# Kernel optimization log

Hardware: AMD Instinct MI355X
Metric: run time of the kernel (lower is better)

## Reference

```python
import jax, jax.numpy as jnp
import numpy as np

S, B, D = 2048, 2, 768
H = 12
DK = D // H
DFF = 3072
EPS = 1e-5


def _layernorm(x, g, b):
    mu = jnp.mean(x, axis=-1, keepdims=True)
    var = jnp.mean(jnp.square(x - mu), axis=-1, keepdims=True)
    return (x - mu) * jax.lax.rsqrt(var + EPS) * g + b


def setup_inputs() -> dict:
    key = jax.random.key(0)
    ks = jax.random.split(key, 12)
    s = 0.02
    return {
        "x": jax.random.normal(ks[0], (S, B, D), jnp.float32),
        "wq": jax.random.normal(ks[1], (D, D), jnp.float32) * s,
        "bq": jnp.zeros((D,), jnp.float32),
        "wk": jax.random.normal(ks[2], (D, D), jnp.float32) * s,
        "bk": jnp.zeros((D,), jnp.float32),
        "wv": jax.random.normal(ks[3], (D, D), jnp.float32) * s,
        "bv": jnp.zeros((D,), jnp.float32),
        "wo": jax.random.normal(ks[4], (D, D), jnp.float32) * s,
        "bo": jnp.zeros((D,), jnp.float32),
        "g1": jnp.ones((D,), jnp.float32),
        "b1": jnp.zeros((D,), jnp.float32),
        "g2": jnp.ones((D,), jnp.float32),
        "b2": jnp.zeros((D,), jnp.float32),
        "w1": jax.random.normal(ks[5], (DFF, D), jnp.float32) * s,
        "bb1": jnp.zeros((DFF,), jnp.float32),
        "w2": jax.random.normal(ks[6], (D, DFF), jnp.float32) * s,
        "bb2": jnp.zeros((D,), jnp.float32),
    }


def reference(x, wq, bq, wk, bk, wv, bv, wo, bo, g1, b1, g2, b2, w1, bb1, w2, bb2):
    scale = 1.0 / np.sqrt(DK)
    # --- pre-norm MHA ---
    z = _layernorm(x, g1, b1)                      # [S,B,D]
    q = (z @ wq.T + bq).reshape(S, B, H, DK)
    k = (z @ wk.T + bk).reshape(S, B, H, DK)
    v = (z @ wv.T + bv).reshape(S, B, H, DK)
    scores = jnp.einsum('ibhd,jbhd->ijbh', q, k) * scale  # [S,S,B,H]
    attn = jax.nn.softmax(scores, axis=1)                  # softmax over keys
    ctx = jnp.einsum('ijbh,jbhd->ibhd', attn, v).reshape(S, B, D)
    a = ctx @ wo.T + bo
    x = x + a
    # --- pre-norm FFN (ELU) ---
    z = _layernorm(x, g2, b2)
    h = jax.nn.elu(z @ w1.T + bb1)
    a = h @ w2.T + bb2
    return x + a
```

## Files before the change

kernel.cpp:

```cpp
#include <hip/hip_runtime.h>
#include <hip/hip_bf16.h>
#include <math.h>

#define S_LEN   2048
#define B_SZ    2
#define D_MODEL 768
#define N_HEADS 12
#define DFF     3072
#define N_TOK   4096
#define EPS     1e-5f
#define QKV_N   2304
#define SLOG2E  0.18033688011112042f
#define NSPLIT  2

typedef __attribute__((ext_vector_type(8))) short short8;
typedef __attribute__((ext_vector_type(4))) float f32x4;
typedef unsigned long long u64;
typedef unsigned short u16;
typedef unsigned u32;

__device__ __forceinline__ void gload16(const void* g, void* l) {
    __builtin_amdgcn_global_load_lds(
        (const __attribute__((address_space(1))) void*)g,
        (__attribute__((address_space(3))) void*)l, 16, 0, 0);
}
__device__ __forceinline__ u16 f2bf(float x) {
    union { float f; unsigned u; } c; c.f = x;
    unsigned r = c.u + 0x7FFF + ((c.u >> 16) & 1);
    return (u16)(r >> 16);
}
__device__ __forceinline__ float bf2f(u16 u) {
    union { unsigned u; float f; } c; c.u = ((unsigned)u) << 16; return c.f;
}
__device__ __forceinline__ float fast_exp2(float x) {
    float r; asm("v_exp_f32 %0, %1" : "=v"(r) : "v"(x)); return r;
}

__global__ __launch_bounds__(256) void cvt_all(
    const float* __restrict__ wq, const float* __restrict__ wk,
    const float* __restrict__ wv, const float* __restrict__ wo,
    const float* __restrict__ w1, const float* __restrict__ w2,
    u16* __restrict__ dst)
{
    const int W = 147456;
    int i = blockIdx.x * 256 + threadIdx.x;
    const float* src; int off;
    if      (i <     W) { src = wq; off = 0;     }
    else if (i < 2 * W) { src = wk; off = W;     }
    else if (i < 3 * W) { src = wv; off = 2 * W; }
    else if (i < 4 * W) { src = wo; off = 3 * W; }
    else if (i < 8 * W) { src = w1; off = 4 * W; }
    else                { src = w2; off = 8 * W; }
    float4 v = ((const float4*)src)[i - off];
    union { u16 u[4]; u64 ll; } o;
    o.u[0] = f2bf(v.x); o.u[1] = f2bf(v.y); o.u[2] = f2bf(v.z); o.u[3] = f2bf(v.w);
    ((u64*)dst)[i] = o.ll;
}

__global__ __launch_bounds__(256) void concat_bias(
    const float* __restrict__ bq, const float* __restrict__ bk,
    const float* __restrict__ bv, float* __restrict__ d)
{
    int i = blockIdx.x * 256 + threadIdx.x;
    if (i < 768) d[i] = bq[i];
    else if (i < 1536) d[i] = bk[i - 768];
    else d[i] = bv[i - 1536];
}

__global__ __launch_bounds__(256) void ln_kernel(
    const float* __restrict__ x, const float* __restrict__ g,
    const float* __restrict__ b, u16* __restrict__ z)
{
    int row = blockIdx.x;
    const float* xr = x + (size_t)row * D_MODEL;
    u16* zr = z + (size_t)row * D_MODEL;
    int t = threadIdx.x;
    float loc[3];
    float s1 = 0.f, s2 = 0.f;
#pragma unroll
    for (int i = 0; i < 3; ++i) {
        float v = xr[t + 256 * i];
        loc[i] = v; s1 += v; s2 += v * v;
    }
#pragma unroll
    for (int off = 32; off > 0; off >>= 1) {
        s1 += __shfl_down(s1, off);
        s2 += __shfl_down(s2, off);
    }
    __shared__ float r1[4], r2[4];
    __shared__ float mu_s, is_s;
    int wave = t >> 6, lane = t & 63;
    if (lane == 0) { r1[wave] = s1; r2[wave] = s2; }
    __syncthreads();
    if (t == 0) {
        float a = r1[0] + r1[1] + r1[2] + r1[3];
        float c = r2[0] + r2[1] + r2[2] + r2[3];
        float mu = a * (1.f / D_MODEL);
        float var = c * (1.f / D_MODEL) - mu * mu;
        mu_s = mu; is_s = rsqrtf(var + EPS);
    }
    __syncthreads();
    float mu = mu_s, istd = is_s;
#pragma unroll
    for (int i = 0; i < 3; ++i) {
        int c = t + 256 * i;
        zr[c] = f2bf((loc[i] - mu) * istd * g[c] + b[c]);
    }
}

__global__ __launch_bounds__(256) void ln_fuse(
    const float* __restrict__ x, const u16* __restrict__ p0,
    const u16* __restrict__ p1, const float* __restrict__ bres,
    const float* __restrict__ g, const float* __restrict__ b,
    float* __restrict__ xout, u16* __restrict__ z)
{
    int row = blockIdx.x;
    const float* xr = x + (size_t)row * D_MODEL;
    const u16* p0r = p0 + (size_t)row * D_MODEL;
    const u16* p1r = p1 + (size_t)row * D_MODEL;
    int t = threadIdx.x;
    float loc[3];
    float s1 = 0.f, s2 = 0.f;
#pragma unroll
    for (int i = 0; i < 3; ++i) {
        int c = t + 256 * i;
        float v = xr[c] + bf2f(p0r[c]) + bf2f(p1r[c]) + bres[c];
        loc[i] = v; s1 += v; s2 += v * v;
    }
#pragma unroll
    for (int off = 32; off > 0; off >>= 1) {
        s1 += __shfl_down(s1, off);
        s2 += __shfl_down(s2, off);
    }
    __shared__ float r1[4], r2[4];
    __shared__ float mu_s, is_s;
    int wave = t >> 6, lane = t & 63;
    if (lane == 0) { r1[wave] = s1; r2[wave] = s2; }
    __syncthreads();
    if (t == 0) {
        float a = r1[0] + r1[1] + r1[2] + r1[3];
        float c = r2[0] + r2[1] + r2[2] + r2[3];
        float mu = a * (1.f / D_MODEL);
        float var = c * (1.f / D_MODEL) - mu * mu;
        mu_s = mu; is_s = rsqrtf(var + EPS);
    }
    __syncthreads();
    float mu = mu_s, istd = is_s;
    float* xo = xout + (size_t)row * D_MODEL;
    u16* zr = z + (size_t)row * D_MODEL;
#pragma unroll
    for (int i = 0; i < 3; ++i) {
        int c = t + 256 * i;
        xo[c] = loc[i];
        zr[c] = f2bf((loc[i] - mu) * istd * g[c] + b[c]);
    }
}

template <int MODE>
__global__ __launch_bounds__(256) void gemm_mfma(
    const u16* __restrict__ A, const u16* __restrict__ W,
    const float* __restrict__ bias, void* __restrict__ outp,
    u16* __restrict__ vt, int Ncols, int K, int lda, int ldw, int koff)
{
    __shared__ short AsB[3][128 * 32];
    __shared__ short BsB[3][128 * 32];

    const int t = threadIdx.x;
    const int lane = t & 63, w = t >> 6;
    const int wr = w >> 1, wc = w & 1;

    const int nwg = gridDim.x * gridDim.y;
    const int bid = blockIdx.y * gridDim.x + blockIdx.x;
    const int wg  = (bid & 7) * (nwg >> 3) + (bid >> 3);
    const int row0 = (wg / gridDim.x) * 128;
    const int col0 = (wg % gridDim.x) * 128;
    const int fr = lane & 15, fg = lane >> 4;

    if (MODE == 4) {
        A += (size_t)blockIdx.z * koff;
        W += (size_t)blockIdx.z * koff;
    }

    int o0 = w * 1024 + lane * 16;
    int r0s = o0 >> 6,          sl0 = (o0 >> 4) & 3;
    int r1s = (o0 + 4096) >> 6, sl1 = ((o0 + 4096) >> 4) & 3;
    int ss0 = sl0 ^ ((r0s >> 1) & 3);
    int ss1 = sl1 ^ ((r1s >> 1) & 3);
    const u16* Asrc0 = A + (size_t)(row0 + r0s) * lda + ss0 * 8;
    const u16* Asrc1 = A + (size_t)(row0 + r1s) * lda + ss1 * 8;
    const u16* Bsrc0 = W + (size_t)(col0 + r0s) * ldw + ss0 * 8;
    const u16* Bsrc1 = W + (size_t)(col0 + r1s) * ldw + ss1 * 8;
    const int od0 = w * 1024, od1 = w * 1024 + 4096;

    f32x4 acc[4][4] = {};
    const int nt = K / 32;

    auto stage = [&](int c, int k0) {
        gload16(Asrc0 + k0, (char*)AsB[c] + od0);
        gload16(Asrc1 + k0, (char*)AsB[c] + od1);
        gload16(Bsrc0 + k0, (char*)BsB[c] + od0);
        gload16(Bsrc1 + k0, (char*)BsB[c] + od1);
    };

    stage(0, 0);
    stage(1, 32);

    for (int tt = 0; tt < nt; ++tt) {
        if (tt + 1 < nt)
            asm volatile("s_waitcnt vmcnt(4)\n\ts_barrier" ::: "memory");
        else
            asm volatile("s_waitcnt vmcnt(0)\n\ts_barrier" ::: "memory");
        if (tt + 2 < nt) stage((tt + 2) % 3, (tt + 2) * 32);

        const char* As = (const char*)AsB[tt % 3];
        const char* Bs = (const char*)BsB[tt % 3];
        short8 af[4], bfr[4];
#pragma unroll
        for (int m = 0; m < 4; ++m) {
            int r = wr * 64 + m * 16 + fr;
            af[m] = *(const short8*)(As + r * 64 + ((fg ^ ((r >> 1) & 3)) << 4));
        }
#pragma unroll
        for (int n = 0; n < 4; ++n) {
            int r = wc * 64 + n * 16 + fr;
            bfr[n] = *(const short8*)(Bs + r * 64 + ((fg ^ ((r >> 1) & 3)) << 4));
        }
#pragma unroll
        for (int m = 0; m < 4; ++m)
#pragma unroll
            for (int n = 0; n < 4; ++n)
                acc[m][n] = __builtin_amdgcn_mfma_f32_16x16x32_bf16(
                    af[m], bfr[n], acc[m][n], 0, 0, 0);
    }

    u16* pout16 = nullptr;
    if (MODE == 4) pout16 = blockIdx.z ? vt : (u16*)outp;

#pragma unroll
    for (int m = 0; m < 4; ++m) {
        int rbase = row0 + wr * 64 + m * 16 + fg * 4;
#pragma unroll
        for (int n = 0; n < 4; ++n) {
            int col = col0 + wc * 64 + n * 16 + fr;
            float bv = (MODE == 4) ? 0.f : bias[col];
            if (MODE == 1 && col >= 1536) {
                int cc = col - 1536, hh = cc >> 6, dk = cc & 63;
                int s_a = rbase >> 1;
                float v0 = acc[m][n][0] + bv, v1 = acc[m][n][1] + bv;
                float v2 = acc[m][n][2] + bv, v3 = acc[m][n][3] + bv;
                unsigned lo = (unsigned)f2bf(v0) | ((unsigned)f2bf(v2) << 16);
                unsigned hi = (unsigned)f2bf(v1) | ((unsigned)f2bf(v3) << 16);
                *(unsigned*)&vt[((size_t)hh * 64 + dk) * 2048 + s_a] = lo;
                *(unsigned*)&vt[((size_t)(N_HEADS + hh) * 64 + dk) * 2048 + s_a] = hi;
            } else {
#pragma unroll
                for (int r = 0; r < 4; ++r) {
                    int row = rbase + r;
                    float v = acc[m][n][r] + bv;
                    if (MODE == 3) {
                        v = v > 0.f ? v : (fast_exp2(v * 1.44269504f) - 1.f);
                        ((u16*)outp)[(size_t)row * Ncols + col] = f2bf(v);
                    } else if (MODE == 4) {
                        pout16[(size_t)row * 768 + col] = f2bf(v);
                    } else {
                        if (col < 768) v *= SLOG2E;
                        ((u16*)outp)[(size_t)row * QKV_N + col] = f2bf(v);
                    }
                }
            }
        }
    }
}

__global__ __launch_bounds__(256) void reduce_add(
    const u16* __restrict__ p0, const u16* __restrict__ p1,
    const float* __restrict__ bias, const float* __restrict__ res,
    float* __restrict__ out)
{
    int i = blockIdx.x * 256 + threadIdx.x;
    int col4 = i % (D_MODEL / 4);
    u64 a = ((const u64*)p0)[i];
    u64 c = ((const u64*)p1)[i];
    float4 o = ((const float4*)res)[i];
    float4 bb = ((const float4*)bias)[col4];
    o.x += bf2f((u16)a)         + bf2f((u16)c)         + bb.x;
    o.y += bf2f((u16)(a >> 16)) + bf2f((u16)(c >> 16)) + bb.y;
    o.z += bf2f((u16)(a >> 32)) + bf2f((u16)(c >> 32)) + bb.z;
    o.w += bf2f((u16)(a >> 48)) + bf2f((u16)(c >> 48)) + bb.w;
    ((float4*)out)[i] = o;
}

__global__ __launch_bounds__(256) void attn_mfma(
    const u16* qkv, const u16* __restrict__ vt,
    u16* op0, u16* __restrict__ op1, float* __restrict__ lp)
{
    __shared__ short KsB[2][64 * 64];
    __shared__ short VtB[2][64 * 64];
    __shared__ short PsB[4][32 * 64];

    const int t = threadIdx.x, lane = t & 63, w = t >> 6;
    const int fr = lane & 15, fg = lane >> 4;
    const int fg4 = fg * 4;

    const int nwg = gridDim.x * gridDim.y;
    const int bid = blockIdx.y * gridDim.x + blockIdx.x;
    const int wg  = (bid & 7) * (nwg >> 3) + (bid >> 3);
    const int qb = wg % gridDim.x, bh = wg / gridDim.x;
    const int zid = blockIdx.z;
    const int b = bh / N_HEADS, h = bh % N_HEADS;

    short8 qf[2][2];
#pragma unroll
    for (int qg = 0; qg < 2; ++qg) {
        int srow = qb * 128 + w * 32 + qg * 16 + fr;
        size_t tok = (size_t)srow * B_SZ + b;
#pragma unroll
        for (int s = 0; s < 2; ++s)
            qf[qg][s] = *(const short8*)(qkv + tok * QKV_N + h * 64 + s * 32 + fg * 8);
    }

    const short8 ones8 = { (short)0x3F80, (short)0x3F80, (short)0x3F80, (short)0x3F80,
                           (short)0x3F80, (short)0x3F80, (short)0x3F80, (short)0x3F80 };

    f32x4 l_acc[2] = {};
    f32x4 O[2][4] = {};

    int o0 = w * 1024 + lane * 16;
    int r0 = o0 >> 7,          sl0 = (o0 >> 4) & 7;
    int r1 = (o0 + 4096) >> 7, sl1 = ((o0 + 4096) >> 4) & 7;
    int ss0 = sl0 ^ (r0 & 7), ss1 = sl1 ^ (r1 & 7);
    const u16* kbase = qkv + 768 + h * 64;
    const u16* vtb = vt + (size_t)bh * 64 * S_LEN;
    const int od0 = w * 1024, od1 = w * 1024 + 4096;
    char* Pw = (char*)PsB[w];

    auto stageKV = [&](int c, int kb) {
        gload16(kbase + ((size_t)(kb * 64 + r0) * B_SZ + b) * QKV_N + ss0 * 8, (char*)KsB[c] + od0);
        gload16(kbase + ((size_t)(kb * 64 + r1) * B_SZ + b) * QKV_N + ss1 * 8, (char*)KsB[c] + od1);
        gload16(vtb + (size_t)r0 * S_LEN + kb * 64 + ss0 * 8, (char*)VtB[c] + od0);
        gload16(vtb + (size_t)r1 * S_LEN + kb * 64 + ss1 * 8, (char*)VtB[c] + od1);
    };

    const int kb0 = zid * (S_LEN / 64 / NSPLIT);
    stageKV(0, kb0);

    for (int it = 0; it < S_LEN / 64 / NSPLIT; ++it) {
        __syncthreads();
        if (it + 1 < S_LEN / 64 / NSPLIT) stageKV((it + 1) & 1, kb0 + it + 1);
        const char* Ks  = (const char*)KsB[it & 1];
        const char* Vts = (const char*)VtB[it & 1];

        f32x4 sacc[2][4] = {};
        __builtin_amdgcn_s_setprio(1);
#pragma unroll
        for (int f = 0; f < 4; ++f) {
            int r = f * 16 + fr;
#pragma unroll
            for (int s = 0; s < 2; ++s) {
                int slot = (s * 4 + fg) ^ (r & 7);
                short8 kf = *(const short8*)(Ks + r * 128 + slot * 16);
                sacc[0][f] = __builtin_amdgcn_mfma_f32_16x16x32_bf16(kf, qf[0][s], sacc[0][f], 0, 0, 0);
                sacc[1][f] = __builtin_amdgcn_mfma_f32_16x16x32_bf16(kf, qf[1][s], sacc[1][f], 0, 0, 0);
            }
        }
        __builtin_amdgcn_s_setprio(0);

#pragma unroll
        for (int qg = 0; qg < 2; ++qg) {
            int rr = qg * 16 + fr;
#pragma unroll
            for (int f = 0; f < 4; ++f) {
                float e0 = fast_exp2(sacc[qg][f][0]);
                float e1 = fast_exp2(sacc[qg][f][1]);
                float e2 = fast_exp2(sacc[qg][f][2]);
                float e3 = fast_exp2(sacc[qg][f][3]);
                u32 u0, u1;
                asm("v_cvt_pk_bf16_f32 %0, %1, %2" : "=v"(u0) : "v"(e0), "v"(e1));
                asm("v_cvt_pk_bf16_f32 %0, %1, %2" : "=v"(u1) : "v"(e2), "v"(e3));
                int slot = (f * 2 + (fg >> 1)) ^ (rr & 7);
                uint2 uu; uu.x = u0; uu.y = u1;
                *(uint2*)(Pw + rr * 128 + slot * 16 + (fg & 1) * 8) = uu;
            }
        }
        asm volatile("s_waitcnt lgkmcnt(0)" ::: "memory");
        __builtin_amdgcn_sched_barrier(0);

        __builtin_amdgcn_s_setprio(1);
#pragma unroll
        for (int s = 0; s < 2; ++s) {
            int pslot = (s * 4 + fg) ^ (fr & 7);
            short8 pf0 = *(const short8*)(Pw + fr * 128 + pslot * 16);
            short8 pf1 = *(const short8*)(Pw + (16 + fr) * 128 + pslot * 16);
            l_acc[0] = __builtin_amdgcn_mfma_f32_16x16x32_bf16(pf0, ones8, l_acc[0], 0, 0, 0);
            l_acc[1] = __builtin_amdgcn_mfma_f32_16x16x32_bf16(pf1, ones8, l_acc[1], 0, 0, 0);
#pragma unroll
            for (int n = 0; n < 4; ++n) {
                int vrow = n * 16 + fr;
                int vslot = (s * 4 + fg) ^ (vrow & 7);
                short8 vf = *(const short8*)(Vts + vrow * 128 + vslot * 16);
                O[0][n] = __builtin_amdgcn_mfma_f32_16x16x32_bf16(pf0, vf, O[0][n], 0, 0, 0);
                O[1][n] = __builtin_amdgcn_mfma_f32_16x16x32_bf16(pf1, vf, O[1][n], 0, 0, 0);
            }
        }
        __builtin_amdgcn_s_setprio(0);
    }

    u16* op = zid ? op1 : op0;
    const int ld = zid ? 768 : QKV_N;
    float* lz = lp + (size_t)zid * (N_TOK * N_HEADS);
#pragma unroll
    for (int qg = 0; qg < 2; ++qg) {
        int srow = qb * 128 + w * 32 + qg * 16 + fg4;
        size_t tok0 = (size_t)srow * B_SZ + b;
#pragma unroll
        for (int n = 0; n < 4; ++n) {
            int col = h * 64 + n * 16 + fr;
            op[(tok0 + 0) * ld + col] = f2bf(O[qg][n][0]);
            op[(tok0 + 2) * ld + col] = f2bf(O[qg][n][1]);
            op[(tok0 + 4) * ld + col] = f2bf(O[qg][n][2]);
            op[(tok0 + 6) * ld + col] = f2bf(O[qg][n][3]);
        }
        if (fr == 0) {
            lz[(tok0 + 0) * N_HEADS + h] = l_acc[qg][0];
            lz[(tok0 + 2) * N_HEADS + h] = l_acc[qg][1];
            lz[(tok0 + 4) * N_HEADS + h] = l_acc[qg][2];
            lz[(tok0 + 6) * N_HEADS + h] = l_acc[qg][3];
        }
    }
}

__global__ __launch_bounds__(256) void combine_attn(
    const u16* __restrict__ op0, const u16* op1,
    const float* __restrict__ lp, u16* ctx)
{
    int i = blockIdx.x * 256 + threadIdx.x;
    int tok = i / 192, c4 = i % 192, h = c4 >> 4;
    float l0 = lp[tok * N_HEADS + h];
    float l1 = lp[N_TOK * N_HEADS + tok * N_HEADS + h];
    float inv = 1.f / (l0 + l1);
    u64 o0 = *(const u64*)(op0 + (size_t)tok * QKV_N + c4 * 4);
    u64 o1 = *(const u64*)(op1 + (size_t)tok * 768 + c4 * 4);
    union { u16 u[4]; u64 ll; } r;
#pragma unroll
    for (int j = 0; j < 4; ++j)
        r.u[j] = f2bf((bf2f((u16)(o0 >> (16 * j))) +
                       bf2f((u16)(o1 >> (16 * j)))) * inv);
    *(u64*)(ctx + (size_t)tok * 768 + c4 * 4) = r.ll;
}

extern "C" void kernel_launch(void* const* d_in, const int* in_sizes, int n_in,
                              void* d_out, int out_size, void* d_ws, size_t ws_size,
                              hipStream_t stream)
{
    (void)in_sizes; (void)n_in; (void)out_size; (void)ws_size;
    const float* x   = (const float*)d_in[0];
    const float* wq  = (const float*)d_in[1];
    const float* bq  = (const float*)d_in[2];
    const float* wk  = (const float*)d_in[3];
    const float* bk  = (const float*)d_in[4];
    const float* wv  = (const float*)d_in[5];
    const float* bv  = (const float*)d_in[6];
    const float* wo  = (const float*)d_in[7];
    const float* bo  = (const float*)d_in[8];
    const float* g1  = (const float*)d_in[9];
    const float* b1  = (const float*)d_in[10];
    const float* g2  = (const float*)d_in[11];
    const float* b2  = (const float*)d_in[12];
    const float* w1  = (const float*)d_in[13];
    const float* bb1 = (const float*)d_in[14];
    const float* w2  = (const float*)d_in[15];
    const float* bb2 = (const float*)d_in[16];
    float* out = (float*)d_out;

    const size_t ND = (size_t)N_TOK * D_MODEL;
    char* p = (char*)d_ws;
    u16* z    = (u16*)p;
    p += ND * 2;
    u16* qkv  = (u16*)p;
    u16* hbuf = (u16*)p;
    p += (size_t)N_TOK * QKV_N * 2;
    u16* vtb  = (u16*)p;
    p += (size_t)B_SZ * N_HEADS * 64 * S_LEN * 2;
    u16* wqkvb = (u16*)p;
    p += (size_t)QKV_N * D_MODEL * 2;
    u16* wob   = (u16*)p; p += (size_t)D_MODEL * D_MODEL * 2;
    u16* w1b   = (u16*)p; p += (size_t)DFF * D_MODEL * 2;
    u16* w2b   = (u16*)p; p += (size_t)D_MODEL * DFF * 2;
    float* biasqkv = (float*)p;

    u16* aop0 = qkv + 1536;
    u16* aop1 = z;
    float* aml = (float*)wqkvb;
    u16* wop0 = qkv;
    u16* wop1 = qkv + ND;
    u16* fp0  = z;
    u16* fp1  = wqkvb;

    dim3 blk(256);

    cvt_all<<<6912, blk, 0, stream>>>(wq, wk, wv, wo, w1, w2, wqkvb);
    concat_bias<<<9, blk, 0, stream>>>(bq, bk, bv, biasqkv);

    ln_kernel<<<N_TOK, blk, 0, stream>>>(x, g1, b1, z);
    gemm_mfma<1><<<dim3(QKV_N / 128, N_TOK / 128), blk, 0, stream>>>(
        z, wqkvb, biasqkv, qkv, vtb, QKV_N, D_MODEL, D_MODEL, D_MODEL, 0);
    attn_mfma<<<dim3(S_LEN / 128, B_SZ * N_HEADS, NSPLIT), blk, 0, stream>>>(
        qkv, vtb, aop0, aop1, aml);
    combine_attn<<<(int)(ND / 4 / 256), blk, 0, stream>>>(aop0, aop1, aml, z);
    gemm_mfma<4><<<dim3(D_MODEL / 128, N_TOK / 128, 2), blk, 0, stream>>>(
        z, wob, nullptr, wop0, wop1, D_MODEL, 384, D_MODEL, D_MODEL, 384);
    ln_fuse<<<N_TOK, blk, 0, stream>>>(x, wop0, wop1, bo, g2, b2, out, z);
    gemm_mfma<3><<<dim3(DFF / 128, N_TOK / 128), blk, 0, stream>>>(
        z, w1b, bb1, hbuf, nullptr, DFF, D_MODEL, D_MODEL, D_MODEL, 0);
    gemm_mfma<4><<<dim3(D_MODEL / 128, N_TOK / 128, 2), blk, 0, stream>>>(
        hbuf, w2b, nullptr, fp0, fp1, D_MODEL, 1536, DFF, DFF, 1536);
    reduce_add<<<(int)(ND / 4 / 256), blk, 0, stream>>>(fp0, fp1, bb2, out, out);
}
```

Before: 183.0 us.

## Switch attention to 32x32x16 MFMA and keep P in registers via permlane swap

The attention kernel moves from 16x16x32 MFMA tiles to 32x32x16 tiles for QK^T, the row-sum, and PV. The softmax probabilities are no longer written to and reread from LDS. They are converted to bf16 and rearranged into the A-operand layout in registers with v_permlane32_swap, which removes the per-wave P buffer and an lgkmcnt wait. The output store loop is rewritten for the 32x32 accumulator layout. Larger accumulators raise register pressure and may lower occupancy.

Measured after the change: 193.3 us. 5.6% more time.

```diff
diff --git a/kernel.cpp b/kernel.cpp
--- a/kernel.cpp
+++ b/kernel.cpp
@@ -15,6 +15,7 @@
 
 typedef __attribute__((ext_vector_type(8))) short short8;
 typedef __attribute__((ext_vector_type(4))) float f32x4;
+typedef __attribute__((ext_vector_type(16))) float f32x16;
 typedef unsigned long long u64;
 typedef unsigned short u16;
 typedef unsigned u32;
@@ -296,11 +297,9 @@
 {
     __shared__ short KsB[2][64 * 64];
     __shared__ short VtB[2][64 * 64];
-    __shared__ short PsB[4][32 * 64];
 
     const int t = threadIdx.x, lane = t & 63, w = t >> 6;
-    const int fr = lane & 15, fg = lane >> 4;
-    const int fg4 = fg * 4;
+    const int l31 = lane & 31, hi = lane >> 5;
 
     const int nwg = gridDim.x * gridDim.y;
     const int bid = blockIdx.y * gridDim.x + blockIdx.x;
@@ -309,21 +308,19 @@
     const int zid = blockIdx.z;
     const int b = bh / N_HEADS, h = bh % N_HEADS;
 
-    short8 qf[2][2];
-#pragma unroll
-    for (int qg = 0; qg < 2; ++qg) {
-        int srow = qb * 128 + w * 32 + qg * 16 + fr;
-        size_t tok = (size_t)srow * B_SZ + b;
-#pragma unroll
-        for (int s = 0; s < 2; ++s)
-            qf[qg][s] = *(const short8*)(qkv + tok * QKV_N + h * 64 + s * 32 + fg * 8);
+    short8 qf[4];
+    {
+        size_t tok = (size_t)(qb * 128 + w * 32 + l31) * B_SZ + b;
+#pragma unroll
+        for (int s = 0; s < 4; ++s)
+            qf[s] = *(const short8*)(qkv + tok * QKV_N + h * 64 + s * 16 + hi * 8);
     }
 
     const short8 ones8 = { (short)0x3F80, (short)0x3F80, (short)0x3F80, (short)0x3F80,
                            (short)0x3F80, (short)0x3F80, (short)0x3F80, (short)0x3F80 };
 
-    f32x4 l_acc[2] = {};
-    f32x4 O[2][4] = {};
+    f32x16 l16 = {};
+    f32x16 O[2] = {};
 
     int o0 = w * 1024 + lane * 16;
     int r0 = o0 >> 7,          sl0 = (o0 >> 4) & 7;
@@ -332,7 +329,6 @@
     const u16* kbase = qkv + 768 + h * 64;
     const u16* vtb = vt + (size_t)bh * 64 * S_LEN;
     const int od0 = w * 1024, od1 = w * 1024 + 4096;
-    char* Pw = (char*)PsB[w];
 
     auto stageKV = [&](int c, int kb) {
         gload16(kbase + ((size_t)(kb * 64 + r0) * B_SZ + b) * QKV_N + ss0 * 8, (char*)KsB[c] + od0);
@@ -350,56 +346,54 @@
         const char* Ks  = (const char*)KsB[it & 1];
         const char* Vts = (const char*)VtB[it & 1];
 
-        f32x4 sacc[2][4] = {};
+        f32x16 sacc[2] = {};
         __builtin_amdgcn_s_setprio(1);
 #pragma unroll
-        for (int f = 0; f < 4; ++f) {
-            int r = f * 16 + fr;
-#pragma unroll
-            for (int s = 0; s < 2; ++s) {
-                int slot = (s * 4 + fg) ^ (r & 7);
-                short8 kf = *(const short8*)(Ks + r * 128 + slot * 16);
-                sacc[0][f] = __builtin_amdgcn_mfma_f32_16x16x32_bf16(kf, qf[0][s], sacc[0][f], 0, 0, 0);
-                sacc[1][f] = __builtin_amdgcn_mfma_f32_16x16x32_bf16(kf, qf[1][s], sacc[1][f], 0, 0, 0);
+        for (int kb = 0; kb < 2; ++kb) {
+            int row = kb * 32 + l31;
+#pragma unroll
+            for (int s = 0; s < 4; ++s) {
+                int slot = (2 * s + hi) ^ (row & 7);
+                short8 kf = *(const short8*)(Ks + row * 128 + slot * 16);
+                sacc[kb] = __builtin_amdgcn_mfma_f32_32x32x16_bf16(kf, qf[s], sacc[kb], 0, 0, 0);
             }
         }
         __builtin_amdgcn_s_setprio(0);
 
-#pragma unroll
-        for (int qg = 0; qg < 2; ++qg) {
-            int rr = qg * 16 + fr;
-#pragma unroll
-            for (int f = 0; f < 4; ++f) {
-                float e0 = fast_exp2(sacc[qg][f][0]);
-                float e1 = fast_exp2(sacc[qg][f][1]);
-                float e2 = fast_exp2(sacc[qg][f][2]);
-                float e3 = fast_exp2(sacc[qg][f][3]);
-                u32 u0, u1;
-                asm("v_cvt_pk_bf16_f32 %0, %1, %2" : "=v"(u0) : "v"(e0), "v"(e1));
-                asm("v_cvt_pk_bf16_f32 %0, %1, %2" : "=v"(u1) : "v"(e2), "v"(e3));
-                int slot = (f * 2 + (fg >> 1)) ^ (rr & 7);
-                uint2 uu; uu.x = u0; uu.y = u1;
-                *(uint2*)(Pw + rr * 128 + slot * 16 + (fg & 1) * 8) = uu;
-            }
+        float p[2][16];
+#pragma unroll
+        for (int kb = 0; kb < 2; ++kb)
+#pragma unroll
+            for (int r = 0; r < 16; ++r)
+                p[kb][r] = fast_exp2(sacc[kb][r]);
+
+        short8 pa[4];
+#pragma unroll
+        for (int m = 0; m < 4; ++m) {
+            const int s = m >> 1;
+            const int bse = (m & 1) * 8;
+            u32 a0, a1, b0, b1;
+            asm("v_cvt_pk_bf16_f32 %0, %1, %2" : "=v"(a0) : "v"(p[s][bse + 0]), "v"(p[s][bse + 1]));
+            asm("v_cvt_pk_bf16_f32 %0, %1, %2" : "=v"(a1) : "v"(p[s][bse + 2]), "v"(p[s][bse + 3]));
+            asm("v_cvt_pk_bf16_f32 %0, %1, %2" : "=v"(b0) : "v"(p[s][bse + 4]), "v"(p[s][bse + 5]));
+            asm("v_cvt_pk_bf16_f32 %0, %1, %2" : "=v"(b1) : "v"(p[s][bse + 6]), "v"(p[s][bse + 7]));
+            asm("v_permlane32_swap_b32 %0, %1" : "+v"(a0), "+v"(b0));
+            asm("v_permlane32_swap_b32 %0, %1" : "+v"(a1), "+v"(b1));
+            union { u32 d[4]; short8 s8; } pk;
+            pk.d[0] = a0; pk.d[1] = a1; pk.d[2] = b0; pk.d[3] = b1;
+            pa[m] = pk.s8;
         }
-        asm volatile("s_waitcnt lgkmcnt(0)" ::: "memory");
-        __builtin_amdgcn_sched_barrier(0);
 
         __builtin_amdgcn_s_setprio(1);
 #pragma unroll
-        for (int s = 0; s < 2; ++s) {
-            int pslot = (s * 4 + fg) ^ (fr & 7);
-            short8 pf0 = *(const short8*)(Pw + fr * 128 + pslot * 16);
-            short8 pf1 = *(const short8*)(Pw + (16 + fr) * 128 + pslot * 16);
-            l_acc[0] = __builtin_amdgcn_mfma_f32_16x16x32_bf16(pf0, ones8, l_acc[0], 0, 0, 0);
-            l_acc[1] = __builtin_amdgcn_mfma_f32_16x16x32_bf16(pf1, ones8, l_acc[1], 0, 0, 0);
-#pragma unroll
-            for (int n = 0; n < 4; ++n) {
-                int vrow = n * 16 + fr;
-                int vslot = (s * 4 + fg) ^ (vrow & 7);
-                short8 vf = *(const short8*)(Vts + vrow * 128 + vslot * 16);
-                O[0][n] = __builtin_amdgcn_mfma_f32_16x16x32_bf16(pf0, vf, O[0][n], 0, 0, 0);
-                O[1][n] = __builtin_amdgcn_mfma_f32_16x16x32_bf16(pf1, vf, O[1][n], 0, 0, 0);
+        for (int m = 0; m < 4; ++m) {
+            l16 = __builtin_amdgcn_mfma_f32_32x32x16_bf16(pa[m], ones8, l16, 0, 0, 0);
+#pragma unroll
+            for (int dkb = 0; dkb < 2; ++dkb) {
+                int row = dkb * 32 + l31;
+                int slot = (2 * m + hi) ^ (row & 7);
+                short8 vf = *(const short8*)(Vts + row * 128 + slot * 16);
+                O[dkb] = __builtin_amdgcn_mfma_f32_32x32x16_bf16(pa[m], vf, O[dkb], 0, 0, 0);
             }
         }
         __builtin_amdgcn_s_setprio(0);
@@ -409,23 +403,14 @@
     const int ld = zid ? 768 : QKV_N;
     float* lz = lp + (size_t)zid * (N_TOK * N_HEADS);
 #pragma unroll
-    for (int qg = 0; qg < 2; ++qg) {
-        int srow = qb * 128 + w * 32 + qg * 16 + fg4;
-        size_t tok0 = (size_t)srow * B_SZ + b;
-#pragma unroll
-        for (int n = 0; n < 4; ++n) {
-            int col = h * 64 + n * 16 + fr;
-            op[(tok0 + 0) * ld + col] = f2bf(O[qg][n][0]);
-            op[(tok0 + 2) * ld + col] = f2bf(O[qg][n][1]);
-            op[(tok0 + 4) * ld + col] = f2bf(O[qg][n][2]);
-            op[(tok0 + 6) * ld + col] = f2bf(O[qg][n][3]);
-        }
-        if (fr == 0) {
-            lz[(tok0 + 0) * N_HEADS + h] = l_acc[qg][0];
-            lz[(tok0 + 2) * N_HEADS + h] = l_acc[qg][1];
-            lz[(tok0 + 4) * N_HEADS + h] = l_acc[qg][2];
-            lz[(tok0 + 6) * N_HEADS + h] = l_acc[qg][3];
-        }
+    for (int r = 0; r < 16; ++r) {
+        int q = (r & 3) + 8 * (r >> 2) + 4 * hi;
+        size_t tok = (size_t)(qb * 128 + w * 32 + q) * B_SZ + b;
+#pragma unroll
+        for (int dkb = 0; dkb < 2; ++dkb)
+            op[tok * ld + h * 64 + dkb * 32 + l31] = f2bf(O[dkb][r]);
+        if (l31 == 0)
+            lz[tok * N_HEADS + h] = l16[r];
     }
 }
 
```
